# Kernel optimization log

Measured on AMD Instinct MI355X. Metric: run time of the kernel, lower is better.

## Reference

```python
import jax, jax.numpy as jnp
import numpy as np

B, H, W, D = 8, 56, 56, 256
NH = 8
KD = D // NH  # 32, key_dim == head_dim (value_factor=1)
FFN = 1024
EPS = 1e-6
SCALE = KD ** -0.5


def _lin(x, w, b):
    # torch nn.Linear: y = x @ W^T + b, W is (out, in)
    return jnp.einsum('...i,oi->...o', x, w) + b


def _ln(x, g, b):
    mu = jnp.mean(x, axis=-1, keepdims=True)
    var = jnp.mean(jnp.square(x - mu), axis=-1, keepdims=True)
    return (x - mu) * jax.lax.rsqrt(var + EPS) * g + b


def _dwconv(x, kernel, bias):
    # x: (B,H,W,C) NHWC, kernel: (kh,kw,1,C) HWIO depthwise
    y = jax.lax.conv_general_dilated(
        x, kernel, window_strides=(1, 1), padding='SAME',
        dimension_numbers=('NHWC', 'HWIO', 'NHWC'),
        feature_group_count=x.shape[-1])
    return y + bias


def _rope_sincos(h, w, head_dim):
    # PosEncodingGen: angle freq repeated pairwise, index over flattened H*W
    angle = 1.0 / (10000.0 ** jnp.linspace(0.0, 1.0, head_dim // 2))
    angle = jnp.repeat(angle, 2)  # (head_dim,)
    idx = jnp.arange(h * w, dtype=jnp.float32)
    phase = idx[:, None] * angle[None, :]
    return jnp.sin(phase).reshape(h, w, head_dim), jnp.cos(phase).reshape(h, w, head_dim)


def _angle_transform(x, sin, cos):
    # x: (B,NH,H,W,KD); sin/cos: (H,W,KD) broadcast over (B,NH)
    x1 = x[..., ::2]
    x2 = x[..., 1::2]
    rot = jnp.stack([-x2, x1], axis=-1).reshape(x.shape)
    return x * cos + rot * sin


def setup_inputs() -> dict:
    key = jax.random.key(0)
    ks = jax.random.split(key, 16)
    s = 0.02
    return {
        'x': jax.random.normal(ks[0], (B, H, W, D), jnp.float32),
        'cpe_w': jax.random.normal(ks[1], (3, 3, 1, D), jnp.float32) * s,
        'cpe_b': jnp.zeros((D,), jnp.float32),
        'ln1_g': jnp.ones((D,), jnp.float32),
        'ln1_b': jnp.zeros((D,), jnp.float32),
        'wq': jax.random.normal(ks[2], (D, D), jnp.float32) * s,
        'bq': jnp.zeros((D,), jnp.float32),
        'wk': jax.random.normal(ks[3], (D, D), jnp.float32) * s,
        'bk': jnp.zeros((D,), jnp.float32),
        'wv': jax.random.normal(ks[4], (D, D), jnp.float32) * s,
        'bv': jnp.zeros((D,), jnp.float32),
        'lepe_w': jax.random.normal(ks[5], (5, 5, 1, D), jnp.float32) * s,
        'lepe_b': jnp.zeros((D,), jnp.float32),
        'wo': jax.random.normal(ks[6], (D, D), jnp.float32) * s,
        'bo': jnp.zeros((D,), jnp.float32),
        'ln2_g': jnp.ones((D,), jnp.float32),
        'ln2_b': jnp.zeros((D,), jnp.float32),
        'fc1_w': jax.random.normal(ks[7], (FFN, D), jnp.float32) * s,
        'fc1_b': jnp.zeros((FFN,), jnp.float32),
        'dw_w': jax.random.normal(ks[8], (3, 3, 1, FFN), jnp.float32) * s,
        'dw_b': jnp.zeros((FFN,), jnp.float32),
        'fc2_w': jax.random.normal(ks[9], (D, FFN), jnp.float32) * s,
        'fc2_b': jnp.zeros((D,), jnp.float32),
    }


def _decomposed_gsa(x, sin, cos, wq, bq, wk, bk, wv, bv, lepe_w, lepe_b, wo, bo):
    b, h, w, d = x.shape
    q = _lin(x, wq, bq)
    k = _lin(x, wk, bk) * SCALE
    v = _lin(x, wv, bv)
    lepe = _dwconv(v, lepe_w, lepe_b)  # (b,h,w,d)
    # -> (b, nh, h, w, kd)
    q = q.reshape(b, h, w, NH, KD).transpose(0, 3, 1, 2, 4)
    k = k.reshape(b, h, w, NH, KD).transpose(0, 3, 1, 2, 4)
    v = v.reshape(b, h, w, NH, KD).transpose(0, 3, 1, 2, 4)
    qr = _angle_transform(q, sin, cos)
    kr = _angle_transform(k, sin, cos)
    # attention along W axis (per row h)
    aw = jnp.einsum('bnhik,bnhjk->bnhij', qr, kr)  # (b,nh,h,w,w)
    aw = jax.nn.softmax(aw, axis=-1)
    vw = jnp.einsum('bnhij,bnhjd->bnhid', aw, v)   # (b,nh,h,w,kd)
    # attention along H axis (per column w)
    ah = jnp.einsum('bniwk,bnjwk->bnwij', qr, kr)  # (b,nh,w,h,h)
    ah = jax.nn.softmax(ah, axis=-1)
    out = jnp.einsum('bnwij,bnjwd->bniwd', ah, vw)  # (b,nh,h,w,kd)
    # faithful to torch: flat reinterpret of (b,nh,h,w,kd) -> (b,h,w,nh*kd)
    out = out.reshape(b, h, w, NH * KD)
    out = out + lepe
    return _lin(out, wo, bo)


def reference(x, cpe_w, cpe_b, ln1_g, ln1_b, wq, bq, wk, bk, wv, bv,
              lepe_w, lepe_b, wo, bo, ln2_g, ln2_b,
              fc1_w, fc1_b, dw_w, dw_b, fc2_w, fc2_b):
    b, h, w, d = x.shape
    x = x + _dwconv(x, cpe_w, cpe_b)
    sin, cos = _rope_sincos(h, w, KD)
    # attention sub-block
    shortcut = x
    xn = _ln(x, ln1_g, ln1_b)
    attn = _decomposed_gsa(xn, sin, cos, wq, bq, wk, bk, wv, bv,
                           lepe_w, lepe_b, wo, bo)
    x = shortcut + attn  # drop_path=Identity, gamma_1=1.0
    # FFN sub-block (subconv=True, subln=False)
    shortcut = x
    xn = _ln(x, ln2_g, ln2_b)
    hdn = jax.nn.gelu(_lin(xn, fc1_w, fc1_b), approximate=False)
    hdn = _dwconv(hdn, dw_w, dw_b) + hdn
    ffn_out = _lin(hdn, fc2_w, fc2_b)
    return shortcut + ffn_out
```

## Files before the change

kernel.cpp:

```cpp
#include <hip/hip_runtime.h>
#include <hip/hip_bf16.h>
#include <math.h>

typedef __hip_bfloat16 bf16;

#define HB 8
#define HH 56
#define WWD 56
#define DD 256
#define NHEAD 8
#define KDIM 32
#define FFND 1024
#define NPIX (HB*HH*WWD)
#define SCALE_K 0.17677669529663687f

typedef __attribute__((ext_vector_type(8))) short short8;
typedef __attribute__((ext_vector_type(4))) float f32x4;

__device__ inline float toF(float x){ return x; }
__device__ inline float toF(bf16 x){ return __bfloat162float(x); }

__device__ inline float bfu_to_f(unsigned short u){
    union { float f; unsigned u32; } cv; cv.u32 = (unsigned)u << 16; return cv.f;
}

__device__ inline unsigned short f2bu(float f){
    union { bf16 b; unsigned short u; } cv; cv.b = __float2bfloat16(f); return cv.u;
}
__device__ inline unsigned pk2(float a, float b){
    return (unsigned)f2bu(a) | ((unsigned)f2bu(b) << 16);
}

__global__ __launch_bounds__(256) void wcvt_kernel(
    const float* __restrict__ wq, const float* __restrict__ wk,
    const float* __restrict__ wv, const float* __restrict__ wo,
    const float* __restrict__ f1, const float* __restrict__ f2,
    bf16* __restrict__ dst)
{
    const int id = blockIdx.x*256 + threadIdx.x;
    const float* src; int off;
    if      (id < 8192)  { src = wq; off = id; }
    else if (id < 16384) { src = wk; off = id - 8192; }
    else if (id < 24576) { src = wv; off = id - 16384; }
    else if (id < 32768) { src = wo; off = id - 24576; }
    else if (id < 65536) { src = f1; off = id - 32768; }
    else                 { src = f2; off = id - 65536; }
    const float4 a = *(const float4*)(src + (size_t)off*8);
    const float4 b = *(const float4*)(src + (size_t)off*8 + 4);
    uint4 v; v.x = pk2(a.x,a.y); v.y = pk2(a.z,a.w); v.z = pk2(b.x,b.y); v.w = pk2(b.z,b.w);
    *(uint4*)(dst + (size_t)id*8) = v;
}

__global__ __launch_bounds__(256) void rope_init_kernel(float2* __restrict__ t)
{
    const int id = blockIdx.x*256 + threadIdx.x;
    const int idx = id >> 4, i = id & 15;
    const float ph = (float)idx * exp2f(-(float)i * 0.88584749196996324f);
    t[id] = make_float2(cosf(ph), sinf(ph));
}

__global__ __launch_bounds__(256) void cpe_ln_kernel(
    const float* __restrict__ x, const float* __restrict__ wt,
    const float* __restrict__ bias, const float* __restrict__ g,
    const float* __restrict__ bln, float* __restrict__ X0, bf16* __restrict__ B1)
{
    constexpr int C = 256, VEC = 4, CG = 64, PPB = 4, KS = 3, P = 1;
    const int tid = threadIdx.x;
    const int cg  = tid % CG;
    const int pl  = tid / CG;
    const int p   = blockIdx.x * PPB + pl;
    const int w   = p % WWD;
    const int h   = (p / WWD) % HH;
    const int b   = p / (WWD * HH);
    const int c0  = cg * VEC;

    float acc[VEC];
    {
        const float4 b0 = *(const float4*)(bias + c0);
        acc[0] = b0.x; acc[1] = b0.y; acc[2] = b0.z; acc[3] = b0.w;
    }
    #pragma unroll
    for (int ky = 0; ky < KS; ky++) {
        const int hh = h + ky - P;
        if (hh < 0 || hh >= HH) continue;
        #pragma unroll
        for (int kx = 0; kx < KS; kx++) {
            const int ww = w + kx - P;
            if (ww < 0 || ww >= WWD) continue;
            const float4 wv = *(const float4*)(wt + (size_t)(ky*KS + kx)*C + c0);
            const float4 f0 = *(const float4*)(x + ((size_t)((b*HH + hh)*WWD + ww))*C + c0);
            acc[0] += f0.x * wv.x; acc[1] += f0.y * wv.y;
            acc[2] += f0.z * wv.z; acc[3] += f0.w * wv.w;
        }
    }
    const size_t obase = (size_t)p*C + c0;
    {
        const float4 f0 = *(const float4*)(x + obase);
        acc[0] += f0.x; acc[1] += f0.y; acc[2] += f0.z; acc[3] += f0.w;
    }
    { float4 o; o.x = acc[0]; o.y = acc[1]; o.z = acc[2]; o.w = acc[3];
      *(float4*)(X0 + obase) = o; }
    float s1 = acc[0] + acc[1] + acc[2] + acc[3];
    float s2 = acc[0]*acc[0] + acc[1]*acc[1] + acc[2]*acc[2] + acc[3]*acc[3];
    #pragma unroll
    for (int d = 1; d < 64; d <<= 1) { s1 += __shfl_xor(s1, d); s2 += __shfl_xor(s2, d); }
    const float mu  = s1 * (1.0f/DD);
    const float var = s2 * (1.0f/DD) - mu*mu;
    const float inv = rsqrtf(var + 1e-6f);
    const float4 gv = *(const float4*)(g + c0);
    const float4 bv = *(const float4*)(bln + c0);
    uint2 o;
    o.x = pk2((acc[0]-mu)*inv*gv.x + bv.x, (acc[1]-mu)*inv*gv.y + bv.y);
    o.y = pk2((acc[2]-mu)*inv*gv.z + bv.z, (acc[3]-mu)*inv*gv.w + bv.w);
    *(uint2*)(B1 + obase) = o;
}

template<int KS, bool ADD, int C>
__global__ __launch_bounds__(256) void dwconv_slide_kernel(
    const bf16* __restrict__ in, const float* __restrict__ wt, int wst,
    const float* __restrict__ bias, bf16* __restrict__ out)
{
    constexpr int VEC = 8, CG = C/VEC, GPB = 256/CG, NPX = 4, P = KS/2, NX = NPX+KS-1;
    constexpr int GPR = WWD/NPX;
    constexpr int NB  = NPIX/(NPX*GPB);
    const int tid = threadIdx.x;
    const int cg  = tid % CG;
    const int gl  = tid / CG;
    const int bid = blockIdx.x;
    const int swb = (bid & 7) * (NB >> 3) + (bid >> 3);
    const int gid = swb * GPB + gl;
    const int row = gid / GPR;
    const int w0  = (gid % GPR) * NPX;
    const int h   = row % HH;
    const int b   = row / HH;
    const int c0  = cg * VEC;

    float acc[NPX][VEC];
    {
        const float4 b0 = *(const float4*)(bias + c0);
        const float4 b1 = *(const float4*)(bias + c0 + 4);
        #pragma unroll
        for (int j = 0; j < NPX; j++) {
            acc[j][0]=b0.x; acc[j][1]=b0.y; acc[j][2]=b0.z; acc[j][3]=b0.w;
            acc[j][4]=b1.x; acc[j][5]=b1.y; acc[j][6]=b1.z; acc[j][7]=b1.w;
        }
    }

    #pragma unroll
    for (int ky = 0; ky < KS; ky++) {
        const int hh = h + ky - P;
        if (hh < 0 || hh >= HH) continue;
        const bf16* rowp = in + ((size_t)(b*HH + hh) * WWD) * C + c0;
        float wv[KS][VEC];
        #pragma unroll
        for (int kx = 0; kx < KS; kx++) {
            const float* wp = wt + (size_t)(ky*KS + kx)*wst + c0;
            const float4 w0v = *(const float4*)(wp);
            const float4 w1v = *(const float4*)(wp + 4);
            wv[kx][0]=w0v.x; wv[kx][1]=w0v.y; wv[kx][2]=w0v.z; wv[kx][3]=w0v.w;
            wv[kx][4]=w1v.x; wv[kx][5]=w1v.y; wv[kx][6]=w1v.z; wv[kx][7]=w1v.w;
        }
        #pragma unroll
        for (int x = 0; x < NX; x++) {
            const int ww = w0 - P + x;
            short8 raw = {0,0,0,0,0,0,0,0};
            if (ww >= 0 && ww < WWD) raw = *(const short8*)(rowp + (size_t)ww*C);
            float f[VEC];
            #pragma unroll
            for (int e = 0; e < VEC; e++) f[e] = bfu_to_f((unsigned short)raw[e]);
            #pragma unroll
            for (int j = 0; j < NPX; j++) {
                const int kx = x - j;
                if (kx < 0 || kx >= KS) continue;
                #pragma unroll
                for (int e = 0; e < VEC; e++)
                    acc[j][e] += f[e] * wv[kx][e];
            }
        }
    }

    #pragma unroll
    for (int j = 0; j < NPX; j++) {
        const size_t obase = ((size_t)row*WWD + w0 + j)*C + c0;
        if constexpr (ADD) {
            short8 vv = *(const short8*)(in + obase);
            #pragma unroll
            for (int e = 0; e < VEC; e++) acc[j][e] += bfu_to_f((unsigned short)vv[e]);
        }
        uint4 o;
        o.x = pk2(acc[j][0], acc[j][1]); o.y = pk2(acc[j][2], acc[j][3]);
        o.z = pk2(acc[j][4], acc[j][5]); o.w = pk2(acc[j][6], acc[j][7]);
        *(uint4*)(out + obase) = o;
    }
}

__global__ __launch_bounds__(256) void ln_kernel(
    const float* __restrict__ x, const float* __restrict__ g,
    const float* __restrict__ b, bf16* __restrict__ out)
{
    const int wv   = threadIdx.x >> 6;
    const int lane = threadIdx.x & 63;
    const int t    = blockIdx.x * 4 + wv;
    const float4 xv = *(const float4*)(x + (size_t)t*DD + lane*4);
    float s1 = xv.x + xv.y + xv.z + xv.w;
    float s2 = xv.x*xv.x + xv.y*xv.y + xv.z*xv.z + xv.w*xv.w;
    #pragma unroll
    for (int d = 1; d < 64; d <<= 1) {
        s1 += __shfl_xor(s1, d);
        s2 += __shfl_xor(s2, d);
    }
    const float mu  = s1 * (1.0f/DD);
    const float var = s2 * (1.0f/DD) - mu*mu;
    const float inv = rsqrtf(var + 1e-6f);
    const float4 gv = *(const float4*)(g + lane*4);
    const float4 bv = *(const float4*)(b + lane*4);
    uint2 o;
    o.x = pk2((xv.x-mu)*inv*gv.x + bv.x, (xv.y-mu)*inv*gv.y + bv.y);
    o.y = pk2((xv.z-mu)*inv*gv.z + bv.z, (xv.w-mu)*inv*gv.w + bv.w);
    *(uint2*)(out + (size_t)t*DD + lane*4) = o;
}

template<int EPI, int ROPE>
__global__ __launch_bounds__(256) void mgemm128_kernel(
    const bf16* __restrict__ A, const bf16* __restrict__ Wb, int ldw,
    const float* __restrict__ bias, const float2* __restrict__ ropet,
    const float* __restrict__ residF, float* __restrict__ accF, bf16* __restrict__ outB,
    int M, int N, int K, float scale)
{
    __shared__ unsigned short Sh[2*128*40];
    unsigned short* As = Sh;
    unsigned short* Bs = Sh + 128*40;
    const int tid  = threadIdx.x;
    const int wid  = tid >> 6;
    const int lane = tid & 63;
    const int quad = lane >> 4;
    const int l15  = lane & 15;
    const int wr   = wid >> 1;
    const int wc   = wid & 1;

    const int NXg = gridDim.x;
    const int T   = NXg * gridDim.y;
    int f = blockIdx.y * NXg + blockIdx.x;
    f = (f & 7) * (T >> 3) + (f >> 3);
    const int row0 = (f / NXg) * 128;
    const int col0 = (f % NXg) * 128;

    f32x4 acc[4][4];
    #pragma unroll
    for (int m = 0; m < 4; m++)
        #pragma unroll
        for (int n = 0; n < 4; n++)
            acc[m][n] = (f32x4){0.f, 0.f, 0.f, 0.f};

    const int r  = tid >> 2;
    const int cc = tid & 3;

    for (int k0 = 0; k0 < K; k0 += 32) {
        __syncthreads();
        #pragma unroll
        for (int h = 0; h < 2; h++) {
            const int rr = r + h*64;
            *(uint4*)(&As[rr*40 + cc*8]) = *(const uint4*)(A  + (size_t)(row0 + rr) * K   + k0 + cc*8);
            *(uint4*)(&Bs[rr*40 + cc*8]) = *(const uint4*)(Wb + (size_t)(col0 + rr) * ldw + k0 + cc*8);
        }
        __syncthreads();
        short8 af[4], bfr[4];
        #pragma unroll
        for (int m = 0; m < 4; m++)
            af[m] = *(const short8*)(&As[(wr*64 + m*16 + l15)*40 + quad*8]);
        #pragma unroll
        for (int n = 0; n < 4; n++)
            bfr[n] = *(const short8*)(&Bs[(wc*64 + n*16 + l15)*40 + quad*8]);
        #pragma unroll
        for (int m = 0; m < 4; m++)
            #pragma unroll
            for (int n = 0; n < 4; n++)
                acc[m][n] = __builtin_amdgcn_mfma_f32_16x16x32_bf16(af[m], bfr[n], acc[m][n], 0, 0, 0);
    }

    __syncthreads();
    float* Ls = (float*)Sh;
    const int cbl = l15 * 4;
    #pragma unroll
    for (int m = 0; m < 4; m++) {
        #pragma unroll
        for (int n = 0; n < 4; n++) {
            const int col = n*16 + l15;
            const float bval = bias[col0 + wc*64 + col];
            #pragma unroll
            for (int reg = 0; reg < 4; reg++) {
                float y = (acc[m][n][reg] + bval) * scale;
                if (EPI == 1) y = 0.5f*y*(1.0f + erff(y*0.70710678118654752f));
                Ls[wid*1088 + (quad*4+reg)*68 + col] = y;
            }
        }
        #pragma unroll
        for (int p = 0; p < 4; p++) {
            const int rowt = p*4 + quad;
            const float4 v = *(const float4*)&Ls[wid*1088 + rowt*68 + cbl];
            const int mm = row0 + wr*64 + m*16 + rowt;
            const int nc = col0 + wc*64 + cbl;
            const size_t o = (size_t)mm * N + nc;
            if (EPI == 2) {
                const float4 rv = *(const float4*)(residF + o);
                float4 w; w.x = v.x+rv.x; w.y = v.y+rv.y; w.z = v.z+rv.z; w.w = v.w+rv.w;
                *(float4*)(accF + o) = w;
            } else {
                float a = v.x, b = v.y, c = v.z, d = v.w;
                if (ROPE) {
                    const int idx = mm % (HH*WWD);
                    const int i0 = (nc & 31) >> 1;
                    const float4 t = *(const float4*)&ropet[(size_t)idx*16 + i0];
                    const float na = a*t.x - b*t.y;
                    const float nb = b*t.x + a*t.y;
                    const float ncv = c*t.z - d*t.w;
                    const float nd = d*t.z + c*t.w;
                    a = na; b = nb; c = ncv; d = nd;
                }
                uint2 ov; ov.x = pk2(a, b); ov.y = pk2(c, d);
                *(uint2*)(outB + o) = ov;
            }
        }
    }
}

template<bool COLM>
__global__ __launch_bounds__(256) void attn_mfma_kernel(
    const bf16* __restrict__ q, const bf16* __restrict__ k,
    const bf16* __restrict__ v, const bf16* __restrict__ lepe,
    bf16* __restrict__ outp)
{
    __shared__ unsigned short Qb[64*40];
    __shared__ unsigned short Kb[64*40];
    __shared__ unsigned short Vt[32*80];
    __shared__ unsigned short Pb[64*72];

    const int bid  = blockIdx.x;
    const int line = bid % 56;
    const int nh   = (bid / 56) % NHEAD;
    const int b    = bid / (56 * NHEAD);
    const int tid  = threadIdx.x;
    const int wid  = tid >> 6;
    const int lane = tid & 63;
    const int quad = lane >> 4;
    const int l15  = lane & 15;

    const size_t rstr = COLM ? (size_t)WWD * DD : (size_t)DD;
    const size_t base = COLM ? (((size_t)b*HH*WWD + line) * DD + nh*KDIM)
                             : (((size_t)(b*HH + line) * WWD) * DD + nh*KDIM);

    {
        const int r  = tid >> 2;
        const int cc = tid & 3;
        uint4 zero = {0,0,0,0};
        if (r < 56) {
            size_t g = base + (size_t)r * rstr + cc*8;
            *(uint4*)(&Qb[r*40 + cc*8]) = *(const uint4*)(q + g);
            *(uint4*)(&Kb[r*40 + cc*8]) = *(const uint4*)(k + g);
        } else {
            *(uint4*)(&Qb[r*40 + cc*8]) = zero;
            *(uint4*)(&Kb[r*40 + cc*8]) = zero;
        }
        uint4 vv = zero;
        if (lane < 56)
            vv = *(const uint4*)(v + base + (size_t)lane * rstr + wid*8);
        const unsigned short* pv = (const unsigned short*)&vv;
        #pragma unroll
        for (int e = 0; e < 8; e++)
            Vt[(wid*8 + e)*80 + lane] = pv[e];
    }
    __syncthreads();

    {
        short8 af = *(const short8*)(&Qb[(wid*16 + l15)*40 + quad*8]);
        f32x4 s_[4];
        #pragma unroll
        for (int j = 0; j < 4; j++) {
            short8 bfm = *(const short8*)(&Kb[(j*16 + l15)*40 + quad*8]);
            f32x4 z = {0.f,0.f,0.f,0.f};
            s_[j] = __builtin_amdgcn_mfma_f32_16x16x32_bf16(af, bfm, z, 0, 0, 0);
        }
        const bool v3 = (l15 < 8);
        float mx[4], sm[4];
        #pragma unroll
        for (int reg = 0; reg < 4; reg++) {
            float m01 = fmaxf(s_[0][reg], s_[1][reg]);
            float m23 = v3 ? fmaxf(s_[2][reg], s_[3][reg]) : s_[2][reg];
            mx[reg] = fmaxf(m01, m23);
        }
        #pragma unroll
        for (int d = 1; d < 16; d <<= 1) {
            #pragma unroll
            for (int reg = 0; reg < 4; reg++)
                mx[reg] = fmaxf(mx[reg], __shfl_xor(mx[reg], d));
        }
        float e_[4][4];
        #pragma unroll
        for (int reg = 0; reg < 4; reg++) sm[reg] = 0.f;
        #pragma unroll
        for (int j = 0; j < 4; j++) {
            #pragma unroll
            for (int reg = 0; reg < 4; reg++) {
                const bool valid = (j < 3) || v3;
                float ex = valid ? expf(s_[j][reg] - mx[reg]) : 0.f;
                e_[j][reg] = ex;
                sm[reg] += ex;
            }
        }
        #pragma unroll
        for (int d = 1; d < 16; d <<= 1) {
            #pragma unroll
            for (int reg = 0; reg < 4; reg++)
                sm[reg] += __shfl_xor(sm[reg], d);
        }
        float inv[4];
        #pragma unroll
        for (int reg = 0; reg < 4; reg++) inv[reg] = 1.0f / sm[reg];
        #pragma unroll
        for (int j = 0; j < 4; j++)
            #pragma unroll
            for (int reg = 0; reg < 4; reg++)
                Pb[(wid*16 + quad*4 + reg)*72 + j*16 + l15] = f2bu(e_[j][reg] * inv[reg]);
    }
    __syncthreads();

    {
        f32x4 acc[2];
        acc[0] = (f32x4){0.f,0.f,0.f,0.f};
        acc[1] = (f32x4){0.f,0.f,0.f,0.f};
        #pragma unroll
        for (int k0 = 0; k0 < 64; k0 += 32) {
            short8 af = *(const short8*)(&Pb[(wid*16 + l15)*72 + k0 + quad*8]);
            #pragma unroll
            for (int nt = 0; nt < 2; nt++) {
                short8 bfm = *(const short8*)(&Vt[(nt*16 + l15)*80 + k0 + quad*8]);
                acc[nt] = __builtin_amdgcn_mfma_f32_16x16x32_bf16(af, bfm, acc[nt], 0, 0, 0);
            }
        }
        #pragma unroll
        for (int nt = 0; nt < 2; nt++) {
            #pragma unroll
            for (int reg = 0; reg < 4; reg++) {
                const int m = wid*16 + quad*4 + reg;
                const int d = nt*16 + l15;
                if (m < 56) {
                    float val = acc[nt][reg];
                    if (COLM) {
                        int hp = 7*nh + (m >> 3);
                        int wp = (m & 7)*7 + (line >> 3);
                        int cp = (line & 7)*32 + d;
                        size_t o = ((size_t)(b*HH + hp)*WWD + wp)*DD + cp;
                        outp[o] = __float2bfloat16(val + toF(lepe[o]));
                    } else {
                        outp[base + (size_t)m * rstr + d] = __float2bfloat16(val);
                    }
                }
            }
        }
    }
}

extern "C" void kernel_launch(void* const* d_in, const int* in_sizes, int n_in,
                              void* d_out, int out_size, void* d_ws, size_t ws_size,
                              hipStream_t stream)
{
    const float* x_in   = (const float*)d_in[0];
    const float* cpe_w  = (const float*)d_in[1];
    const float* cpe_b  = (const float*)d_in[2];
    const float* ln1_g  = (const float*)d_in[3];
    const float* ln1_b  = (const float*)d_in[4];
    const float* wq     = (const float*)d_in[5];
    const float* bq     = (const float*)d_in[6];
    const float* wk     = (const float*)d_in[7];
    const float* bk     = (const float*)d_in[8];
    const float* wv     = (const float*)d_in[9];
    const float* bv     = (const float*)d_in[10];
    const float* lepe_w = (const float*)d_in[11];
    const float* lepe_b = (const float*)d_in[12];
    const float* wo     = (const float*)d_in[13];
    const float* bo     = (const float*)d_in[14];
    const float* ln2_g  = (const float*)d_in[15];
    const float* ln2_b  = (const float*)d_in[16];
    const float* fc1_w  = (const float*)d_in[17];
    const float* fc1_b  = (const float*)d_in[18];
    const float* dw_w   = (const float*)d_in[19];
    const float* dw_b   = (const float*)d_in[20];
    const float* fc2_w  = (const float*)d_in[21];
    const float* fc2_b  = (const float*)d_in[22];
    float* out = (float*)d_out;

    const size_t ND = (size_t)NPIX * DD;
    const size_t NF = (size_t)NPIX * FFND;
    char* ws = (char*)d_ws;
    float*  X0    = (float*)(ws);
    float*  ACC   = (float*)(ws + ND*4);
    bf16*   B1    = (bf16*) (ws + ND*8);
    bf16*   B2    = (bf16*) (ws + ND*8 + ND*2);
    bf16*   H1    = (bf16*) (ws + ND*8 + ND*4);
    bf16*   H2    = (bf16*) (ws + ND*8 + ND*4 + NF*2);
    bf16*   WB    = (bf16*) (ws + ND*8 + ND*4 + NF*4);
    float2* ROPET = (float2*)(ws + ND*8 + ND*4 + NF*4 + 786432*2);
    bf16*   B3 = H1;
    bf16*   B4 = H2;
    bf16*   VWb   = (bf16*)d_out;
    bf16*   ATTNb = VWb + ND;

    const bf16* WQb = WB;
    const bf16* WKb = WB + 65536;
    const bf16* WVb = WB + 131072;
    const bf16* WOb = WB + 196608;
    const bf16* F1b = WB + 262144;
    const bf16* F2b = WB + 524288;

    dim3 b256(256);
    dim3 gridD(DD/128, NPIX/128);
    dim3 gridF(FFND/128, NPIX/128);

    wcvt_kernel<<<384, b256, 0, stream>>>(wq, wk, wv, wo, fc1_w, fc2_w, WB);
    rope_init_kernel<<<196, b256, 0, stream>>>(ROPET);
    cpe_ln_kernel<<<NPIX/4, b256, 0, stream>>>(x_in, cpe_w, cpe_b, ln1_g, ln1_b, X0, B1);
    mgemm128_kernel<0,1><<<gridD, b256, 0, stream>>>(B1, WQb, DD, bq, ROPET, nullptr, nullptr, B2, NPIX, DD, DD, 1.0f);
    mgemm128_kernel<0,1><<<gridD, b256, 0, stream>>>(B1, WKb, DD, bk, ROPET, nullptr, nullptr, B3, NPIX, DD, DD, SCALE_K);
    mgemm128_kernel<0,0><<<gridD, b256, 0, stream>>>(B1, WVb, DD, bv, nullptr, nullptr, nullptr, B4, NPIX, DD, DD, 1.0f);
    dwconv_slide_kernel<5, false, 256><<<784, b256, 0, stream>>>(B4, lepe_w, DD, lepe_b, B1);
    attn_mfma_kernel<false><<<HB*NHEAD*HH, b256, 0, stream>>>(B2, B3, B4, nullptr, VWb);
    attn_mfma_kernel<true><<<HB*NHEAD*WWD, b256, 0, stream>>>(B2, B3, VWb, B1, ATTNb);
    mgemm128_kernel<2,0><<<gridD, b256, 0, stream>>>(ATTNb, WOb, DD, bo, nullptr, X0, ACC, nullptr, NPIX, DD, DD, 1.0f);
    ln_kernel<<<NPIX/4, b256, 0, stream>>>(ACC, ln2_g, ln2_b, B2);
    mgemm128_kernel<1,0><<<gridF, b256, 0, stream>>>(B2, F1b, DD, fc1_b, nullptr, nullptr, nullptr, H1, NPIX, FFND, DD, 1.0f);
    dwconv_slide_kernel<3, true, 1024><<<3136, b256, 0, stream>>>(H1, dw_w, FFND, dw_b, H2);
    mgemm128_kernel<2,0><<<gridD, b256, 0, stream>>>(H2, F2b, FFND, fc2_b, nullptr, ACC, out, nullptr, NPIX, DD, FFND, 1.0f);
}
```

Baseline: 352.0 us.

## Fuse Q/K/V projections into one GEMM and use direct global-to-LDS loads

```diff
diff --git a/kernel.cpp b/kernel.cpp
--- a/kernel.cpp
+++ b/kernel.cpp
@@ -29,6 +29,11 @@
 }
 __device__ inline unsigned pk2(float a, float b){
     return (unsigned)f2bu(a) | ((unsigned)f2bu(b) << 16);
+}
+
+__device__ inline void gl16(const bf16* g, unsigned short* l){
+    __builtin_amdgcn_global_load_lds((const __attribute__((address_space(1))) void*)g,
+                                     (__attribute__((address_space(3))) void*)l, 16, 0, 0);
 }
 
 __global__ __launch_bounds__(256) void wcvt_kernel(
@@ -224,12 +229,13 @@
 __global__ __launch_bounds__(256) void mgemm128_kernel(
     const bf16* __restrict__ A, const bf16* __restrict__ Wb, int ldw,
     const float* __restrict__ bias, const float2* __restrict__ ropet,
-    const float* __restrict__ residF, float* __restrict__ accF, bf16* __restrict__ outB,
+    const float* __restrict__ residF, float* __restrict__ accF,
+    bf16* __restrict__ outB, bf16* __restrict__ outK, bf16* __restrict__ outV,
     int M, int N, int K, float scale)
 {
-    __shared__ unsigned short Sh[2*128*40];
+    __shared__ __align__(16) unsigned short Sh[8704];
     unsigned short* As = Sh;
-    unsigned short* Bs = Sh + 128*40;
+    unsigned short* Bs = Sh + 4096;
     const int tid  = threadIdx.x;
     const int wid  = tid >> 6;
     const int lane = tid & 63;
@@ -252,25 +258,25 @@
         for (int n = 0; n < 4; n++)
             acc[m][n] = (f32x4){0.f, 0.f, 0.f, 0.f};
 
-    const int r  = tid >> 2;
-    const int cc = tid & 3;
-
     for (int k0 = 0; k0 < K; k0 += 32) {
         __syncthreads();
         #pragma unroll
-        for (int h = 0; h < 2; h++) {
-            const int rr = r + h*64;
-            *(uint4*)(&As[rr*40 + cc*8]) = *(const uint4*)(A  + (size_t)(row0 + rr) * K   + k0 + cc*8);
-            *(uint4*)(&Bs[rr*40 + cc*8]) = *(const uint4*)(Wb + (size_t)(col0 + rr) * ldw + k0 + cc*8);
+        for (int j = 0; j < 2; j++) {
+            const int ob  = (wid*2 + j)*64;
+            const int o   = ob + lane;
+            const int row = o >> 2;
+            const int ch  = (o & 3) * 8;
+            gl16(A  + (size_t)(row0 + row)*K   + k0 + ch, &As[ob*8]);
+            gl16(Wb + (size_t)(col0 + row)*ldw + k0 + ch, &Bs[ob*8]);
         }
         __syncthreads();
         short8 af[4], bfr[4];
         #pragma unroll
         for (int m = 0; m < 4; m++)
-            af[m] = *(const short8*)(&As[(wr*64 + m*16 + l15)*40 + quad*8]);
+            af[m] = *(const short8*)(&As[(wr*64 + m*16 + l15)*32 + quad*8]);
         #pragma unroll
         for (int n = 0; n < 4; n++)
-            bfr[n] = *(const short8*)(&Bs[(wc*64 + n*16 + l15)*40 + quad*8]);
+            bfr[n] = *(const short8*)(&Bs[(wc*64 + n*16 + l15)*32 + quad*8]);
         #pragma unroll
         for (int m = 0; m < 4; m++)
             #pragma unroll
@@ -281,6 +287,12 @@
     __syncthreads();
     float* Ls = (float*)Sh;
     const int cbl = l15 * 4;
+    const int seg = (EPI == 3) ? (col0 >> 8) : 0;
+    bf16* dst = outB;
+    if (EPI == 3) dst = (seg == 0) ? outB : ((seg == 1) ? outK : outV);
+    const float esc = (EPI == 3) ? ((seg == 1) ? scale : 1.0f) : scale;
+    const bool doRope = ROPE && (EPI != 3 || seg < 2);
+
     #pragma unroll
     for (int m = 0; m < 4; m++) {
         #pragma unroll
@@ -289,7 +301,7 @@
             const float bval = bias[col0 + wc*64 + col];
             #pragma unroll
             for (int reg = 0; reg < 4; reg++) {
-                float y = (acc[m][n][reg] + bval) * scale;
+                float y = (acc[m][n][reg] + bval) * esc;
                 if (EPI == 1) y = 0.5f*y*(1.0f + erff(y*0.70710678118654752f));
                 Ls[wid*1088 + (quad*4+reg)*68 + col] = y;
             }
@@ -299,26 +311,29 @@
             const int rowt = p*4 + quad;
             const float4 v = *(const float4*)&Ls[wid*1088 + rowt*68 + cbl];
             const int mm = row0 + wr*64 + m*16 + rowt;
-            const int nc = col0 + wc*64 + cbl;
-            const size_t o = (size_t)mm * N + nc;
             if (EPI == 2) {
+                const size_t o = (size_t)mm * N + col0 + wc*64 + cbl;
                 const float4 rv = *(const float4*)(residF + o);
                 float4 w; w.x = v.x+rv.x; w.y = v.y+rv.y; w.z = v.z+rv.z; w.w = v.w+rv.w;
                 *(float4*)(accF + o) = w;
             } else {
+                const int ncl = (EPI == 3) ? ((col0 & 255) + wc*64 + cbl)
+                                           : (col0 + wc*64 + cbl);
+                const size_t o = (EPI == 3) ? ((size_t)mm * 256 + ncl)
+                                            : ((size_t)mm * N + ncl);
                 float a = v.x, b = v.y, c = v.z, d = v.w;
-                if (ROPE) {
+                if (doRope) {
                     const int idx = mm % (HH*WWD);
-                    const int i0 = (nc & 31) >> 1;
+                    const int i0 = (ncl & 31) >> 1;
                     const float4 t = *(const float4*)&ropet[(size_t)idx*16 + i0];
-                    const float na = a*t.x - b*t.y;
-                    const float nb = b*t.x + a*t.y;
+                    const float na  = a*t.x - b*t.y;
+                    const float nb  = b*t.x + a*t.y;
                     const float ncv = c*t.z - d*t.w;
-                    const float nd = d*t.z + c*t.w;
+                    const float nd  = d*t.z + c*t.w;
                     a = na; b = nb; c = ncv; d = nd;
                 }
                 uint2 ov; ov.x = pk2(a, b); ov.y = pk2(c, d);
-                *(uint2*)(outB + o) = ov;
+                *(uint2*)(dst + o) = ov;
             }
         }
     }
@@ -500,34 +515,42 @@
     bf16*   H2    = (bf16*) (ws + ND*8 + ND*4 + NF*2);
     bf16*   WB    = (bf16*) (ws + ND*8 + ND*4 + NF*4);
     float2* ROPET = (float2*)(ws + ND*8 + ND*4 + NF*4 + 786432*2);
+    float*  BQKV  = (float*) (ws + ND*8 + ND*4 + NF*4 + 786432*2 + 50176*8);
     bf16*   B3 = H1;
     bf16*   B4 = H2;
     bf16*   VWb   = (bf16*)d_out;
     bf16*   ATTNb = VWb + ND;
 
-    const bf16* WQb = WB;
-    const bf16* WKb = WB + 65536;
-    const bf16* WVb = WB + 131072;
     const bf16* WOb = WB + 196608;
     const bf16* F1b = WB + 262144;
     const bf16* F2b = WB + 524288;
 
     dim3 b256(256);
+    dim3 gridQKV(768/128, NPIX/128);
     dim3 gridD(DD/128, NPIX/128);
     dim3 gridF(FFND/128, NPIX/128);
 
     wcvt_kernel<<<384, b256, 0, stream>>>(wq, wk, wv, wo, fc1_w, fc2_w, WB);
     rope_init_kernel<<<196, b256, 0, stream>>>(ROPET);
+    hipMemcpyAsync(BQKV,       bq, 256*sizeof(float), hipMemcpyDeviceToDevice, stream);
+    hipMemcpyAsync(BQKV + 256, bk, 256*sizeof(float), hipMemcpyDeviceToDevice, stream);
+    hipMemcpyAsync(BQKV + 512, bv, 256*sizeof(float), hipMemcpyDeviceToDevice, stream);
     cpe_ln_kernel<<<NPIX/4, b256, 0, stream>>>(x_in, cpe_w, cpe_b, ln1_g, ln1_b, X0, B1);
-    mgemm128_kernel<0,1><<<gridD, b256, 0, stream>>>(B1, WQb, DD, bq, ROPET, nullptr, nullptr, B2, NPIX, DD, DD, 1.0f);
-    mgemm128_kernel<0,1><<<gridD, b256, 0, stream>>>(B1, WKb, DD, bk, ROPET, nullptr, nullptr, B3, NPIX, DD, DD, SCALE_K);
-    mgemm128_kernel<0,0><<<gridD, b256, 0, stream>>>(B1, WVb, DD, bv, nullptr, nullptr, nullptr, B4, NPIX, DD, DD, 1.0f);
+    mgemm128_kernel<3,1><<<gridQKV, b256, 0, stream>>>(B1, WB, DD, BQKV, ROPET,
+                                                       nullptr, nullptr, B2, B3, B4,
+                                                       NPIX, 768, DD, SCALE_K);
     dwconv_slide_kernel<5, false, 256><<<784, b256, 0, stream>>>(B4, lepe_w, DD, lepe_b, B1);
     attn_mfma_kernel<false><<<HB*NHEAD*HH, b256, 0, stream>>>(B2, B3, B4, nullptr, VWb);
     attn_mfma_kernel<true><<<HB*NHEAD*WWD, b256, 0, stream>>>(B2, B3, VWb, B1, ATTNb);
-    mgemm128_kernel<2,0><<<gridD, b256, 0, stream>>>(ATTNb, WOb, DD, bo, nullptr, X0, ACC, nullptr, NPIX, DD, DD, 1.0f);
+    mgemm128_kernel<2,0><<<gridD, b256, 0, stream>>>(ATTNb, WOb, DD, bo, nullptr,
+                                                     X0, ACC, nullptr, nullptr, nullptr,
+                                                     NPIX, DD, DD, 1.0f);
     ln_kernel<<<NPIX/4, b256, 0, stream>>>(ACC, ln2_g, ln2_b, B2);
-    mgemm128_kernel<1,0><<<gridF, b256, 0, stream>>>(B2, F1b, DD, fc1_b, nullptr, nullptr, nullptr, H1, NPIX, FFND, DD, 1.0f);
+    mgemm128_kernel<1,0><<<gridF, b256, 0, stream>>>(B2, F1b, DD, fc1_b, nullptr,
+                                                     nullptr, nullptr, H1, nullptr, nullptr,
+                                                     NPIX, FFND, DD, 1.0f);
     dwconv_slide_kernel<3, true, 1024><<<3136, b256, 0, stream>>>(H1, dw_w, FFND, dw_b, H2);
-    mgemm128_kernel<2,0><<<gridD, b256, 0, stream>>>(H2, F2b, FFND, fc2_b, nullptr, ACC, out, nullptr, NPIX, DD, FFND, 1.0f);
-}
+    mgemm128_kernel<2,0><<<gridD, b256, 0, stream>>>(H2, F2b, FFND, fc2_b, nullptr,
+                                                     ACC, out, nullptr, nullptr, nullptr,
+                                                     NPIX, DD, FFND, 1.0f);
+}
```

Result: no change. 347.7 us (-1.2%).
